# Performance work log

Measured on AMD Instinct MI355X. Metric: run time of the kernel, lower is better.

The kernel has to match this reference:

```python
import jax, jax.numpy as jnp
import numpy as np

EPSILON = 0.1      # init kwarg epsilon
NUM_STAB = 1e-06   # init kwarg num_stab
B, D, C = 4096, 3072, 10


def setup_inputs() -> dict:
    key = jax.random.key(0)
    k1, k2 = jax.random.split(key)
    data = jax.random.normal(k1, (B, D), dtype=jnp.float32)
    # small scale keeps softmax probs near-uniform -> rho well-conditioned
    W = jax.random.normal(k2, (D, C), dtype=jnp.float32) * 0.02
    return {"data": data, "W": W}


def _probs(logits, c):
    # output = softmax(...) * (1 - c*num_stab) + num_stab  (numerical stabilization)
    p = jax.nn.softmax(logits, axis=-1)
    return p * (1.0 - c * NUM_STAB) + NUM_STAB


def reference(data, W):
    c = W.shape[1]
    m = c - 1

    def g(x):  # x: [D] -> new_output row: [m]
        p = _probs(x @ W, c)
        s = jnp.sqrt(p)
        return 2.0 * s[:m] / (1.0 - s[m])

    # Vectorized Jacobian: replaces the m sequential autograd.grad calls.
    jac = jax.vmap(jax.jacrev(g))(data)            # [B, m, D]

    p = _probs(data @ W, c)                        # [B, C]
    s_m = jnp.sqrt(p[:, m])                        # [B]
    delta = 2.0 * jnp.arccos(jnp.sqrt(p / c).sum(axis=1))   # [B]
    rho = (2.0 * (1.0 - s_m) - p[:, :m].sum(axis=1)) / (1.0 - s_m)  # [B]
    jac_norm = jnp.sqrt(jnp.square(jac).sum(axis=(1, 2)))   # [B] Frobenius norm per sample
    reg = jax.nn.elu(jac_norm - delta / (rho * EPSILON))
    return reg.mean()
```

## Files before the change

### kernel.cpp

```cpp
#include <hip/hip_runtime.h>
#include <math.h>

#define NB 4096
#define ND 3072
#define NC 10
#define NM 9

static constexpr float kEps      = 0.1f;
static constexpr float kNumStab  = 1e-6f;
static constexpr float kAlpha    = 1.0f - (float)NC * kNumStab;
static constexpr float kInvSqrtC = 0.31622776601683794f;

__global__ __launch_bounds__(1024) void gram_zero_kernel(
        const float* __restrict__ W, float* __restrict__ G,
        float* __restrict__ out) {
    __shared__ float Wls[ND * NC];
    __shared__ float part[16][56];

    const int tid  = threadIdx.x;
    const int lane = tid & 63;
    const int wv   = tid >> 6;

    for (int i = tid; i < (ND * NC) / 4; i += 1024) {
        reinterpret_cast<float4*>(Wls)[i] = reinterpret_cast<const float4*>(W)[i];
    }
    __syncthreads();

    float a[55];
    #pragma unroll
    for (int c = 0; c < 55; ++c) a[c] = 0.0f;

    #pragma unroll
    for (int rr = 0; rr < 3; ++rr) {
        const int row = tid + rr * 1024;
        const float* rp = &Wls[row * NC];
        float r[NC];
        #pragma unroll
        for (int h = 0; h < 5; ++h) {
            const float2 v = *reinterpret_cast<const float2*>(rp + 2 * h);
            r[2 * h] = v.x; r[2 * h + 1] = v.y;
        }
        int c = 0;
        #pragma unroll
        for (int i = 0; i < NC; ++i)
            #pragma unroll
            for (int j = i; j < NC; ++j) {
                a[c] = fmaf(r[i], r[j], a[c]);
                ++c;
            }
    }

    #pragma unroll
    for (int c = 0; c < 55; ++c) {
        #pragma unroll
        for (int off = 32; off > 0; off >>= 1) a[c] += __shfl_xor(a[c], off, 64);
    }
    if (lane == 0) {
        #pragma unroll
        for (int c = 0; c < 55; ++c) part[wv][c] = a[c];
    }
    __syncthreads();

    if (tid < 55) {
        float g = 0.0f;
        #pragma unroll
        for (int w = 0; w < 16; ++w) g += part[w][tid];
        int idx = tid, i = 0;
        while (idx >= (NC - i)) { idx -= (NC - i); ++i; }
        const int j = i + idx;
        G[i * NC + j] = g;
        G[j * NC + i] = g;
    }
    if (tid == 1023) out[0] = 0.0f;
}

__global__ __launch_bounds__(512) void jacreg_kernel(
        const float* __restrict__ data, const float* __restrict__ W,
        const float* __restrict__ G, float* __restrict__ out) {
    __shared__ float Wts[NC * ND];
    __shared__ float Gs[100];
    __shared__ float regs[16];

    const int tid  = threadIdx.x;
    const int lane = tid & 63;
    const int wv   = tid >> 6;

    const int s0 = blockIdx.x * 16 + wv * 2;
    const float* __restrict__ r0 = data + (size_t)s0 * ND;
    const float* __restrict__ r1 = r0 + ND;

    float4 x0a = reinterpret_cast<const float4*>(r0)[lane];
    float4 x1a = reinterpret_cast<const float4*>(r1)[lane];
    float4 x0b = reinterpret_cast<const float4*>(r0)[64 + lane];
    float4 x1b = reinterpret_cast<const float4*>(r1)[64 + lane];

    if (tid < 100) Gs[tid] = G[tid];

    for (int i = tid; i < (ND * NC) / 4; i += 512) {
        const float4 w4 = reinterpret_cast<const float4*>(W)[i];
        const float* wp = reinterpret_cast<const float*>(&w4);
        const int e0 = i * 4;
        #pragma unroll
        for (int j = 0; j < 4; ++j) {
            const int e = e0 + j;
            Wts[(e % NC) * ND + (e / NC)] = wp[j];
        }
    }
    __syncthreads();

    float acc[2][NC];
    #pragma unroll
    for (int s = 0; s < 2; ++s)
        #pragma unroll
        for (int k = 0; k < NC; ++k) acc[s][k] = 0.0f;

    for (int it = 0; it < 12; ++it) {
        const int pit = (it + 2 <= 11) ? it + 2 : 11;
        const float4 n0 = reinterpret_cast<const float4*>(r0)[pit * 64 + lane];
        const float4 n1 = reinterpret_cast<const float4*>(r1)[pit * 64 + lane];

        const int dbase = it * 256 + lane * 4;
        #pragma unroll
        for (int k = 0; k < NC; ++k) {
            const float4 wt = *reinterpret_cast<const float4*>(&Wts[k * ND + dbase]);
            acc[0][k] = fmaf(x0a.x, wt.x, acc[0][k]);
            acc[0][k] = fmaf(x0a.y, wt.y, acc[0][k]);
            acc[0][k] = fmaf(x0a.z, wt.z, acc[0][k]);
            acc[0][k] = fmaf(x0a.w, wt.w, acc[0][k]);
            acc[1][k] = fmaf(x1a.x, wt.x, acc[1][k]);
            acc[1][k] = fmaf(x1a.y, wt.y, acc[1][k]);
            acc[1][k] = fmaf(x1a.z, wt.z, acc[1][k]);
            acc[1][k] = fmaf(x1a.w, wt.w, acc[1][k]);
        }
        x0a = x0b; x1a = x1b;
        x0b = n0;  x1b = n1;
    }

    #pragma unroll
    for (int s = 0; s < 2; ++s)
        #pragma unroll
        for (int k = 0; k < NC; ++k) {
            float v = acc[s][k];
            #pragma unroll
            for (int off = 32; off > 0; off >>= 1) v += __shfl_xor(v, off, 64);
            acc[s][k] = v;
        }

    if (lane < 2) {
        float z[NC];
        #pragma unroll
        for (int k = 0; k < NC; ++k) z[k] = (lane == 0) ? acc[0][k] : acc[1][k];

        float zm = z[0];
        #pragma unroll
        for (int k = 1; k < NC; ++k) zm = fmaxf(zm, z[k]);
        float e[NC], Zs = 0.0f;
        #pragma unroll
        for (int k = 0; k < NC; ++k) { e[k] = expf(z[k] - zm); Zs += e[k]; }
        const float inv = 1.0f / Zs;

        float sg[NC], p[NC], sq[NC], u[NC];
        #pragma unroll
        for (int k = 0; k < NC; ++k) {
            sg[k] = e[k] * inv;
            p[k]  = kAlpha * sg[k] + kNumStab;
            sq[k] = sqrtf(p[k]);
            u[k]  = sg[k] / sq[k];
        }
        const float q = 1.0f - sq[NM];

        float v[NC], t = 0.0f;
        #pragma unroll
        for (int k = 0; k < NC; ++k) {
            float a = 0.0f;
            #pragma unroll
            for (int j = 0; j < NC; ++j) a = fmaf(Gs[k * NC + j], sg[j], a);
            v[k] = a;
            t = fmaf(sg[k], a, t);
        }
        const float vM = v[NM], uM = u[NM];
        const float QMM = Gs[NC * NC - 1] - 2.0f * vM + t;

        float sumJ = 0.0f;
        #pragma unroll
        for (int i = 0; i < NM; ++i) {
            const float Qii = Gs[i * NC + i] - 2.0f * v[i] + t;
            const float QiM = Gs[i * NC + NM] - v[i] - vM + t;
            const float r = sq[i] / q;
            sumJ += u[i] * u[i] * Qii
                  + 2.0f * u[i] * uM * r * QiM
                  + uM * uM * r * r * QMM;
        }
        const float jn = (kAlpha / q) * sqrtf(fmaxf(sumJ, 0.0f));

        float ssum = 0.0f;
        #pragma unroll
        for (int k = 0; k < NC; ++k) ssum += sq[k];
        const float ac = fminf(1.0f, fmaxf(-1.0f, ssum * kInvSqrtC));
        const float delta = 2.0f * acosf(ac);

        float psum = 0.0f;
        #pragma unroll
        for (int k = 0; k < NM; ++k) psum += p[k];
        const float rho = (2.0f * q - psum) / q;

        const float a = jn - delta / (rho * kEps);
        regs[wv * 2 + lane] = (a > 0.0f) ? a : expm1f(a);
    }
    __syncthreads();
    if (tid == 0) {
        float bs = 0.0f;
        #pragma unroll
        for (int i = 0; i < 16; ++i) bs += regs[i];
        atomicAdd(out, bs * (1.0f / (float)NB));
    }
}

extern "C" void kernel_launch(void* const* d_in, const int* in_sizes, int n_in,
                              void* d_out, int out_size, void* d_ws, size_t ws_size,
                              hipStream_t stream) {
    const float* data = (const float*)d_in[0];
    const float* W    = (const float*)d_in[1];
    float* out = (float*)d_out;
    float* G   = (float*)d_ws;

    gram_zero_kernel<<<1, 1024, 0, stream>>>(W, G, out);
    jacreg_kernel<<<NB / 16, 512, 0, stream>>>(data, W, G, out);
}
```

Measured before the change: 110.4 us.

## Fuse Gram-matrix computation into main kernel, recomputing W^T W per block

Removes the separate single-block Gram kernel, which was a serial launch with little parallelism. Each of the 256 blocks now computes W^T W redundantly from its shared-memory copy of W, and the output is zeroed with a memset instead. The cost is extra per-block arithmetic, 55 accumulator registers, shuffle reductions and two extra barriers, which may reduce occupancy.

```diff
diff --git a/kernel.cpp b/kernel.cpp
--- a/kernel.cpp
+++ b/kernel.cpp
@@ -11,73 +11,11 @@
 static constexpr float kAlpha    = 1.0f - (float)NC * kNumStab;
 static constexpr float kInvSqrtC = 0.31622776601683794f;
 
-__global__ __launch_bounds__(1024) void gram_zero_kernel(
-        const float* __restrict__ W, float* __restrict__ G,
+__global__ __launch_bounds__(512) void jacreg_fused_kernel(
+        const float* __restrict__ data, const float* __restrict__ W,
         float* __restrict__ out) {
-    __shared__ float Wls[ND * NC];
-    __shared__ float part[16][56];
-
-    const int tid  = threadIdx.x;
-    const int lane = tid & 63;
-    const int wv   = tid >> 6;
-
-    for (int i = tid; i < (ND * NC) / 4; i += 1024) {
-        reinterpret_cast<float4*>(Wls)[i] = reinterpret_cast<const float4*>(W)[i];
-    }
-    __syncthreads();
-
-    float a[55];
-    #pragma unroll
-    for (int c = 0; c < 55; ++c) a[c] = 0.0f;
-
-    #pragma unroll
-    for (int rr = 0; rr < 3; ++rr) {
-        const int row = tid + rr * 1024;
-        const float* rp = &Wls[row * NC];
-        float r[NC];
-        #pragma unroll
-        for (int h = 0; h < 5; ++h) {
-            const float2 v = *reinterpret_cast<const float2*>(rp + 2 * h);
-            r[2 * h] = v.x; r[2 * h + 1] = v.y;
-        }
-        int c = 0;
-        #pragma unroll
-        for (int i = 0; i < NC; ++i)
-            #pragma unroll
-            for (int j = i; j < NC; ++j) {
-                a[c] = fmaf(r[i], r[j], a[c]);
-                ++c;
-            }
-    }
-
-    #pragma unroll
-    for (int c = 0; c < 55; ++c) {
-        #pragma unroll
-        for (int off = 32; off > 0; off >>= 1) a[c] += __shfl_xor(a[c], off, 64);
-    }
-    if (lane == 0) {
-        #pragma unroll
-        for (int c = 0; c < 55; ++c) part[wv][c] = a[c];
-    }
-    __syncthreads();
-
-    if (tid < 55) {
-        float g = 0.0f;
-        #pragma unroll
-        for (int w = 0; w < 16; ++w) g += part[w][tid];
-        int idx = tid, i = 0;
-        while (idx >= (NC - i)) { idx -= (NC - i); ++i; }
-        const int j = i + idx;
-        G[i * NC + j] = g;
-        G[j * NC + i] = g;
-    }
-    if (tid == 1023) out[0] = 0.0f;
-}
-
-__global__ __launch_bounds__(512) void jacreg_kernel(
-        const float* __restrict__ data, const float* __restrict__ W,
-        const float* __restrict__ G, float* __restrict__ out) {
     __shared__ float Wts[NC * ND];
+    __shared__ float gpart[8][56];
     __shared__ float Gs[100];
     __shared__ float regs[16];
 
@@ -93,8 +31,6 @@
     float4 x1a = reinterpret_cast<const float4*>(r1)[lane];
     float4 x0b = reinterpret_cast<const float4*>(r0)[64 + lane];
     float4 x1b = reinterpret_cast<const float4*>(r1)[64 + lane];
-
-    if (tid < 100) Gs[tid] = G[tid];
 
     for (int i = tid; i < (ND * NC) / 4; i += 512) {
         const float4 w4 = reinterpret_cast<const float4*>(W)[i];
@@ -146,6 +82,53 @@
             acc[s][k] = v;
         }
 
+    float gp[55];
+    #pragma unroll
+    for (int c = 0; c < 55; ++c) gp[c] = 0.0f;
+    {
+        const int d0 = tid * 6;
+        #pragma unroll
+        for (int j = 0; j < 3; ++j) {
+            float rk[NC][2];
+            #pragma unroll
+            for (int k = 0; k < NC; ++k) {
+                const float2 v = *reinterpret_cast<const float2*>(
+                    &Wts[k * ND + d0 + 2 * j]);
+                rk[k][0] = v.x; rk[k][1] = v.y;
+            }
+            int c = 0;
+            #pragma unroll
+            for (int a = 0; a < NC; ++a)
+                #pragma unroll
+                for (int b = a; b < NC; ++b) {
+                    gp[c] = fmaf(rk[a][0], rk[b][0], gp[c]);
+                    gp[c] = fmaf(rk[a][1], rk[b][1], gp[c]);
+                    ++c;
+                }
+        }
+    }
+    #pragma unroll
+    for (int c = 0; c < 55; ++c) {
+        #pragma unroll
+        for (int off = 32; off > 0; off >>= 1) gp[c] += __shfl_xor(gp[c], off, 64);
+    }
+    if (lane == 0) {
+        #pragma unroll
+        for (int c = 0; c < 55; ++c) gpart[wv][c] = gp[c];
+    }
+    __syncthreads();
+    if (tid < 55) {
+        float g = 0.0f;
+        #pragma unroll
+        for (int w = 0; w < 8; ++w) g += gpart[w][tid];
+        int idx = tid, i = 0;
+        while (idx >= (NC - i)) { idx -= (NC - i); ++i; }
+        const int j = i + idx;
+        Gs[i * NC + j] = g;
+        Gs[j * NC + i] = g;
+    }
+    __syncthreads();
+
     if (lane < 2) {
         float z[NC];
         #pragma unroll
@@ -222,8 +205,7 @@
     const float* data = (const float*)d_in[0];
     const float* W    = (const float*)d_in[1];
     float* out = (float*)d_out;
-    float* G   = (float*)d_ws;
-
-    gram_zero_kernel<<<1, 1024, 0, stream>>>(W, G, out);
-    jacreg_kernel<<<NB / 16, 512, 0, stream>>>(data, W, G, out);
+
+    hipMemsetAsync(out, 0, sizeof(float), stream);
+    jacreg_fused_kernel<<<NB / 16, 512, 0, stream>>>(data, W, out);
 }
```

Result: faster. 104.2 us (-5.6%).
